# Kernel optimization log

Measured on AMD Instinct MI355X. Metric: run time of the kernel, lower is better.

The kernel has to match this reference:

```python
import jax, jax.numpy as jnp
import numpy as np

B, S, E, H = 4, 2048, 1024, 16
D = E // H  # head dim = 64


def setup_inputs() -> dict:
    key = jax.random.key(0)
    ks = jax.random.split(key, 9)
    sc = 1.0 / np.sqrt(E)
    x = jax.random.normal(ks[0], (B, S, E), dtype=jnp.float32)
    # causal mask: 1 = keep, 0 = masked -> -inf (matches masked_fill(mask==0, -inf))
    mask = jnp.broadcast_to(jnp.tril(jnp.ones((S, S), dtype=jnp.int32)), (B, S, S))
    return {
        "x": x,
        "mask": mask,
        "wq": jax.random.normal(ks[1], (E, E), dtype=jnp.float32) * sc,
        "bq": jax.random.normal(ks[2], (E,), dtype=jnp.float32) * sc,
        "wk": jax.random.normal(ks[3], (E, E), dtype=jnp.float32) * sc,
        "bk": jax.random.normal(ks[4], (E,), dtype=jnp.float32) * sc,
        "wv": jax.random.normal(ks[5], (E, E), dtype=jnp.float32) * sc,
        "bv": jax.random.normal(ks[6], (E,), dtype=jnp.float32) * sc,
        "wo": jax.random.normal(ks[7], (E, E), dtype=jnp.float32) * sc,
        "bo": jax.random.normal(ks[8], (E,), dtype=jnp.float32) * sc,
    }


def reference(x, mask, wq, bq, wk, bk, wv, bv, wo, bo):
    # nn.Linear: y = x @ W^T + b
    def proj(w, b):
        y = jnp.einsum('bse,fe->bsf', x, w) + b
        return y.reshape(B, S, H, D).transpose(0, 2, 1, 3)  # [B,H,S,D]

    q = proj(wq, bq)
    k = proj(wk, bk)
    v = proj(wv, bv)
    denom = jnp.asarray(np.sqrt(D), dtype=x.dtype)
    score = jnp.einsum('bhqd,bhkd->bhqk', q, k) / denom  # [B,H,S,S]
    score = jnp.where(mask[:, None, :, :] == 0, jnp.asarray(-jnp.inf, score.dtype), score)
    attn = jax.nn.softmax(score, axis=-1)
    out = jnp.einsum('bhqk,bhkd->bhqd', attn, v)  # [B,H,S,D]
    out = out.transpose(0, 2, 1, 3).reshape(B, S, E)
    return jnp.einsum('bse,fe->bsf', out, wo) + bo
```

## Files before the change

### kernel.cpp

```cpp
#include <hip/hip_runtime.h>
#include <cstdint>
#include <cstddef>

typedef unsigned short u16;
typedef __bf16 bf16;
typedef bf16 bf16x8 __attribute__((ext_vector_type(8)));
typedef bf16 bf16x4 __attribute__((ext_vector_type(4)));
typedef float f32x4 __attribute__((ext_vector_type(4)));
typedef u16 u16x8 __attribute__((ext_vector_type(8)));
typedef u16 u16x4 __attribute__((ext_vector_type(4)));

#define ASYNC16(g, l) __builtin_amdgcn_global_load_lds( \
    (const __attribute__((address_space(1))) void*)(g), \
    (__attribute__((address_space(3))) void*)(l), 16, 0, 0)

#define FENCE asm volatile("" ::: "memory")
#define BARRIER do { FENCE; __builtin_amdgcn_s_barrier(); FENCE; } while (0)
#define WAITVM(n) asm volatile("s_waitcnt vmcnt(" #n ")" ::: "memory")

__device__ __forceinline__ u16 f2bf(float f) {
  bf16 h = (bf16)f;
  return __builtin_bit_cast(u16, h);
}

__device__ __forceinline__ u16x4 pk4(float a, float b, float c, float d) {
  bf16x4 v = { (bf16)a, (bf16)b, (bf16)c, (bf16)d };
  return __builtin_bit_cast(u16x4, v);
}

__device__ __forceinline__ void store_out(u16* p, float v) { *p = f2bf(v); }
__device__ __forceinline__ void store_out(float* p, float v) { *p = v; }

__device__ __forceinline__ f32x4 mfma16(bf16x8 a, bf16x8 b, f32x4 c) {
  return __builtin_amdgcn_mfma_f32_16x16x32_bf16(a, b, c, 0, 0, 0);
}

__global__ void prep(const float* __restrict__ x,  const float* __restrict__ wq,
                     const float* __restrict__ wk, const float* __restrict__ wv,
                     const float* __restrict__ wo, const float* __restrict__ bq,
                     const float* __restrict__ bk,
                     u16* __restrict__ xb, u16* __restrict__ wqkb,
                     u16* __restrict__ wvb, u16* __restrict__ wob,
                     float* __restrict__ bqk, float scl)
{
  const int bid = blockIdx.x, tid = threadIdx.x;
  if (bid < 8192) {
    int i = bid * 256 + tid;
    float4 v = ((const float4*)x)[i];
    ((u16x4*)xb)[i] = pk4(v.x, v.y, v.z, v.w);
  } else if (bid < 12288) {
    int wsel = (bid - 8192) >> 10;
    int i = ((bid - 8192) & 1023) * 256 + tid;
    const float* src = wsel == 0 ? wq : wsel == 1 ? wk : wsel == 2 ? wv : wo;
    u16* dst = wsel == 0 ? wqkb : wsel == 1 ? wqkb + 1048576 : wsel == 2 ? wvb : wob;
    float s = wsel == 0 ? scl : 1.0f;
    float4 v = ((const float4*)src)[i];
    ((u16x4*)dst)[i] = pk4(v.x * s, v.y * s, v.z * s, v.w * s);
  } else {
    for (int i = tid; i < 1024; i += 256) {
      bqk[i] = bq[i] * scl;
      bqk[1024 + i] = bk[i];
    }
  }
}

template <typename OutT>
__device__ __forceinline__ void gemm128(
    u16* sA, u16* sB,
    const u16* __restrict__ A, const u16* __restrict__ Bm,
    const float* __restrict__ bias_col, const float* __restrict__ bias_row,
    OutT* __restrict__ C, int M, int N, int K, int bm, int bn)
{
  const int tid = threadIdx.x;
  const int w = tid >> 6, lane = tid & 63;
  const int quad = lane >> 4, l15 = lane & 15;
  const int wr = w >> 2, wc = w & 3;

  const int srow = tid >> 3;
  const int sslot = (tid & 7) ^ (srow & 7);
  const u16* gA = A + (size_t)(bm * 128 + srow) * K + sslot * 8;
  const u16* gB = Bm + (size_t)(bn * 256 + srow) * K + sslot * 8;
  u16* dA = sA + tid * 8;
  u16* dB = sB + tid * 8;
  const size_t rK64 = (size_t)64 * K;

  auto stage0 = [&](int c, int kt) {
    const u16* a = gA + kt * 64;
    u16* da = dA + c * 8192;
    ASYNC16(a, da);
    ASYNC16(a + rK64, da + 4096);
    ASYNC16(gB + kt * 64, dB + c * 16384);
  };
  auto stage1 = [&](int c, int kt) {
    const u16* b = gB + kt * 64;
    u16* db = dB + c * 16384;
    ASYNC16(b + rK64,     db + 4096);
    ASYNC16(b + 2 * rK64, db + 8192);
    ASYNC16(b + 3 * rK64, db + 12288);
  };

  f32x4 acc[4][4] = {};
  bf16x8 af[4][2];
  bf16x8 bfr[2][2];

  const int aRow = (wr * 64 + l15) * 64;
  const int bRow = (wc * 64 + l15) * 64;
  const int sw0 = (quad ^ (l15 & 7)) * 8;

#define LDA(SRC) do { \
    _Pragma("unroll") \
    for (int i = 0; i < 4; i++) { \
      af[i][0] = *(const bf16x8*)((SRC) + aRow + i * 1024 + sw0); \
      af[i][1] = *(const bf16x8*)((SRC) + aRow + i * 1024 + (sw0 ^ 32)); \
    } } while (0)

#define LDB(SRC, NH) do { \
    _Pragma("unroll") \
    for (int j = 0; j < 2; j++) { \
      bfr[j][0] = *(const bf16x8*)((SRC) + bRow + ((NH)*2 + j) * 1024 + sw0); \
      bfr[j][1] = *(const bf16x8*)((SRC) + bRow + ((NH)*2 + j) * 1024 + (sw0 ^ 32)); \
    } } while (0)

#define MMQ(NH) do { \
    __builtin_amdgcn_s_setprio(1); \
    _Pragma("unroll") \
    for (int i = 0; i < 4; i++) { \
      acc[i][(NH)*2+0] = mfma16(af[i][0], bfr[0][0], acc[i][(NH)*2+0]); \
      acc[i][(NH)*2+0] = mfma16(af[i][1], bfr[0][1], acc[i][(NH)*2+0]); \
      acc[i][(NH)*2+1] = mfma16(af[i][0], bfr[1][0], acc[i][(NH)*2+1]); \
      acc[i][(NH)*2+1] = mfma16(af[i][1], bfr[1][1], acc[i][(NH)*2+1]); \
    } \
    __builtin_amdgcn_s_setprio(0); \
  } while (0)

  const int NT = K >> 6;

  stage0(0, 0); stage1(0, 0);
  stage0(1, 1); stage1(1, 1);
  WAITVM(6);
  BARRIER;

  for (int t = 0; t < NT; ++t) {
    const int c = t % 3, c2 = (t + 2) % 3;
    const bool more = (t + 2 < NT);
    const u16* SA = sA + c * 8192;
    const u16* SB = sB + c * 16384;

    LDA(SA); LDB(SB, 0);
    if (more) stage0(c2, t + 2);
    BARRIER;
    MMQ(0);
    BARRIER;

    LDB(SB, 1);
    if (more) {
      stage1(c2, t + 2);
      WAITVM(6);
    } else if (t == NT - 2) {
      WAITVM(0);
    }
    BARRIER;
    MMQ(1);
    BARRIER;
  }

#pragma unroll
  for (int nh = 0; nh < 2; nh++) {
#pragma unroll
    for (int j = 0; j < 2; j++) {
      const int cc = bn * 256 + wc * 64 + nh * 32 + j * 16 + l15;
      const float bc = bias_col ? bias_col[cc] : 0.f;
#pragma unroll
      for (int i = 0; i < 4; i++) {
        const int r0 = bm * 128 + wr * 64 + i * 16 + quad * 4;
        f32x4 v = acc[i][nh * 2 + j];
#pragma unroll
        for (int ri = 0; ri < 4; ri++) {
          const float bb = bc + (bias_row ? bias_row[r0 + ri] : 0.f);
          store_out(&C[(size_t)(r0 + ri) * N + cc], v[ri] + bb);
        }
      }
    }
  }
#undef LDA
#undef LDB
#undef MMQ
}

__global__ __launch_bounds__(512, 2) void gemm_qkv(
    const u16* __restrict__ xb, const u16* __restrict__ wqkb,
    const u16* __restrict__ wvb, const float* __restrict__ bqk,
    const float* __restrict__ bv, u16* __restrict__ qk, u16* __restrict__ vt)
{
  __shared__ __align__(16) u16 sA[3 * 8192];
  __shared__ __align__(16) u16 sB[3 * 16384];
  const int id = blockIdx.x;
  if (id < 512) {
    gemm128<u16>(sA, sB, xb, wqkb, bqk, nullptr, qk, 8192, 2048, 1024,
                 id >> 3, id & 7);
  } else {
    const int j = id - 512;
    gemm128<u16>(sA, sB, wvb, xb, nullptr, bv, vt, 1024, 8192, 1024,
                 j & 7, j >> 3);
  }
}

__global__ __launch_bounds__(512, 2) void gemm_out(
    const u16* __restrict__ ctx, const u16* __restrict__ wob,
    const float* __restrict__ bo, float* __restrict__ out)
{
  __shared__ __align__(16) u16 sA[3 * 8192];
  __shared__ __align__(16) u16 sB[3 * 16384];
  const int id = blockIdx.x;
  gemm128<float>(sA, sB, ctx, wob, bo, nullptr, out, 8192, 1024, 1024,
                 id >> 2, id & 3);
}

__global__ __launch_bounds__(512, 2) void fattn(
    const u16* __restrict__ QK, const u16* __restrict__ VT, u16* __restrict__ ctx)
{
  __shared__ u16 Kt[128 * 64];
  __shared__ u16 Vt[64 * 128];
  __shared__ u16 Pt[8 * 32 * 64];

  const int tid = threadIdx.x;
  const int w = tid >> 6, lane = tid & 63;
  const int quad = lane >> 4, l15 = lane & 15;
  const int bx = blockIdx.x, h = blockIdx.y, b = blockIdx.z;
  const int P8[8] = {7, 0, 6, 1, 5, 2, 4, 3};
  const int tq = (b & 2) ? 7 - P8[bx] : P8[bx];
  const int qbase = tq * 256 + w * 32;

  const int kr = tid >> 3, kc = (tid & 7) ^ (kr & 7);
  const int vr = tid >> 4, vc = (tid & 15) ^ (vr & 15);

  const u16* QKb = QK + (size_t)b * 2048 * 2048;
  const u16* Kg = QKb + 1024 + h * 64 + kc * 8;
  const u16* Vg = VT + (size_t)(h * 64) * 8192 + b * 2048 + vc * 8;

  u16* Pw = Pt + w * 2048;

  bf16x8 ones;
#pragma unroll
  for (int j = 0; j < 8; j++) ones[j] = (bf16)1.0f;

  bf16x8 qf[2][2];
#pragma unroll
  for (int mt = 0; mt < 2; mt++)
#pragma unroll
    for (int ks = 0; ks < 2; ks++)
      qf[mt][ks] = *(const bf16x8*)(QKb + (size_t)(qbase + mt * 16 + l15) * 2048 +
                                    h * 64 + ks * 32 + quad * 8);

  f32x4 oacc[4][2] = {};
  f32x4 lacc[2] = {};

  const int tmax = 2 * tq + 1;
  for (int t = 0; t <= tmax; t++) {
    __syncthreads();
#pragma unroll
    for (int s = 0; s < 2; s++) {
      ASYNC16(Kg + (size_t)(t * 128 + s * 64 + kr) * 2048, Kt + (s * 512 + w * 64) * 8);
      ASYNC16(Vg + (size_t)(s * 32 + vr) * 8192 + t * 128,  Vt + (s * 512 + w * 64) * 8);
    }
    __syncthreads();

    f32x4 st[2][8] = {};
#pragma unroll
    for (int ks = 0; ks < 2; ks++) {
      bf16x8 kf[8];
#pragma unroll
      for (int nt = 0; nt < 8; nt++) {
        int row = nt * 16 + l15;
        kf[nt] = *(const bf16x8*)(Kt + (row * 8 + ((ks * 4 + quad) ^ (row & 7))) * 8);
      }
#pragma unroll
      for (int nt = 0; nt < 8; nt++) {
        st[0][nt] = mfma16(kf[nt], qf[0][ks], st[0][nt]);
        st[1][nt] = mfma16(kf[nt], qf[1][ks], st[1][nt]);
      }
    }

    if (t >= 2 * tq) {
#pragma unroll
      for (int mt = 0; mt < 2; mt++) {
        const int qg = qbase + mt * 16 + l15;
#pragma unroll
        for (int nt = 0; nt < 8; nt++)
#pragma unroll
          for (int r = 0; r < 4; r++)
            if (t * 128 + nt * 16 + quad * 4 + r > qg) st[mt][nt][r] = -3e38f;
      }
    }
#pragma unroll
    for (int mt = 0; mt < 2; mt++)
#pragma unroll
      for (int nt = 0; nt < 8; nt++)
#pragma unroll
        for (int r = 0; r < 4; r++)
          st[mt][nt][r] = exp2f(st[mt][nt][r]);

#pragma unroll
    for (int hf = 0; hf < 2; hf++) {
#pragma unroll
      for (int mt = 0; mt < 2; mt++) {
        const int row = mt * 16 + l15;
#pragma unroll
        for (int n2 = 0; n2 < 4; n2++) {
          int nt = hf * 4 + n2;
          u16x4 pk = pk4(st[mt][nt][0], st[mt][nt][1], st[mt][nt][2], st[mt][nt][3]);
          int c = n2 * 2 + (quad >> 1);
          *(u16x4*)(Pw + (row << 6) + ((c ^ (row & 7)) << 3) + ((quad & 1) << 2)) = pk;
        }
      }
#pragma unroll
      for (int ks = 0; ks < 2; ks++) {
        const int c = ks * 4 + quad;
        bf16x8 pf0 = *(const bf16x8*)(Pw + (l15 << 6) + ((c ^ (l15 & 7)) << 3));
        bf16x8 pf1 = *(const bf16x8*)(Pw + ((16 + l15) << 6) + ((c ^ (l15 & 7)) << 3));
        lacc[0] = mfma16(ones, pf0, lacc[0]);
        lacc[1] = mfma16(ones, pf1, lacc[1]);
#pragma unroll
        for (int dt = 0; dt < 4; dt++) {
          int row = dt * 16 + l15;
          bf16x8 vf = *(const bf16x8*)(Vt + (row * 16 + ((hf * 8 + ks * 4 + quad) ^ (row & 15))) * 8);
          oacc[dt][0] = mfma16(vf, pf0, oacc[dt][0]);
          oacc[dt][1] = mfma16(vf, pf1, oacc[dt][1]);
        }
      }
    }
  }

#pragma unroll
  for (int mt = 0; mt < 2; mt++) {
    float rl = 1.0f / lacc[mt][0];
    size_t row = (size_t)b * 2048 + qbase + mt * 16 + l15;
#pragma unroll
    for (int dt = 0; dt < 4; dt++) {
      u16x4 o = pk4(oacc[dt][mt][0] * rl, oacc[dt][mt][1] * rl,
                    oacc[dt][mt][2] * rl, oacc[dt][mt][3] * rl);
      *(u16x4*)(ctx + row * 1024 + h * 64 + dt * 16 + quad * 4) = o;
    }
  }
}

extern "C" void kernel_launch(void* const* d_in, const int* in_sizes, int n_in,
                              void* d_out, int out_size, void* d_ws, size_t ws_size,
                              hipStream_t stream)
{
  const float* x  = (const float*)d_in[0];
  const float* wq = (const float*)d_in[2];
  const float* bq = (const float*)d_in[3];
  const float* wk = (const float*)d_in[4];
  const float* bk = (const float*)d_in[5];
  const float* wv = (const float*)d_in[6];
  const float* bv = (const float*)d_in[7];
  const float* wo = (const float*)d_in[8];
  const float* bo = (const float*)d_in[9];

  const float SCL = 0.125f * 1.44269504088896f;

  char* ws = (char*)d_ws;
  u16*   xb   = (u16*)(ws);
  u16*   ctx  = (u16*)(ws);
  u16*   wqkb = (u16*)(ws + 16777216);
  u16*   wvb  = (u16*)(ws + 20971520);
  u16*   wob  = (u16*)(ws + 23068672);
  float* bqk  = (float*)(ws + 25165824);
  u16*   qk   = (u16*)(ws + 25174016);
  u16*   vt   = (u16*)(ws + 58728448);
  float* out  = (float*)d_out;

  prep<<<12289, 256, 0, stream>>>(x, wq, wk, wv, wo, bq, bk,
                                  xb, wqkb, wvb, wob, bqk, SCL);

  gemm_qkv<<<768, 512, 0, stream>>>(xb, wqkb, wvb, bqk, bv, qk, vt);
  fattn<<<dim3(8, 16, 4), 512, 0, stream>>>(qk, vt, ctx);
  gemm_out<<<256, 512, 0, stream>>>(ctx, wob, bo, out);
}
```

Before: 312.4 us.

## Double-buffer K/V tiles in flash attention and shrink per-warp P staging

```diff
diff --git a/kernel.cpp b/kernel.cpp
--- a/kernel.cpp
+++ b/kernel.cpp
@@ -219,9 +219,9 @@
 __global__ __launch_bounds__(512, 2) void fattn(
     const u16* __restrict__ QK, const u16* __restrict__ VT, u16* __restrict__ ctx)
 {
-  __shared__ u16 Kt[128 * 64];
-  __shared__ u16 Vt[64 * 128];
-  __shared__ u16 Pt[8 * 32 * 64];
+  __shared__ u16 Kt[2][128 * 64];
+  __shared__ u16 Vt[2][64 * 128];
+  __shared__ u16 Pt[8 * 32 * 32];
 
   const int tid = threadIdx.x;
   const int w = tid >> 6, lane = tid & 63;
@@ -238,7 +238,7 @@
   const u16* Kg = QKb + 1024 + h * 64 + kc * 8;
   const u16* Vg = VT + (size_t)(h * 64) * 8192 + b * 2048 + vc * 8;
 
-  u16* Pw = Pt + w * 2048;
+  u16* Pw = Pt + w * 1024;
 
   bf16x8 ones;
 #pragma unroll
@@ -252,18 +252,28 @@
       qf[mt][ks] = *(const bf16x8*)(QKb + (size_t)(qbase + mt * 16 + l15) * 2048 +
                                     h * 64 + ks * 32 + quad * 8);
 
+  auto stage = [&](int bi, int t) {
+#pragma unroll
+    for (int s = 0; s < 2; s++) {
+      ASYNC16(Kg + (size_t)(t * 128 + s * 64 + kr) * 2048, Kt[bi] + (s * 512 + w * 64) * 8);
+      ASYNC16(Vg + (size_t)(s * 32 + vr) * 8192 + t * 128,  Vt[bi] + (s * 512 + w * 64) * 8);
+    }
+  };
+
   f32x4 oacc[4][2] = {};
   f32x4 lacc[2] = {};
 
   const int tmax = 2 * tq + 1;
+  stage(0, 0);
+
   for (int t = 0; t <= tmax; t++) {
-    __syncthreads();
-#pragma unroll
-    for (int s = 0; s < 2; s++) {
-      ASYNC16(Kg + (size_t)(t * 128 + s * 64 + kr) * 2048, Kt + (s * 512 + w * 64) * 8);
-      ASYNC16(Vg + (size_t)(s * 32 + vr) * 8192 + t * 128,  Vt + (s * 512 + w * 64) * 8);
-    }
-    __syncthreads();
+    const int cur = t & 1;
+    if (t < tmax) { stage(cur ^ 1, t + 1); WAITVM(4); }
+    else          { WAITVM(0); }
+    BARRIER;
+
+    const u16* Kc = Kt[cur];
+    const u16* Vc = Vt[cur];
 
     f32x4 st[2][8] = {};
 #pragma unroll
@@ -272,7 +282,7 @@
 #pragma unroll
       for (int nt = 0; nt < 8; nt++) {
         int row = nt * 16 + l15;
-        kf[nt] = *(const bf16x8*)(Kt + (row * 8 + ((ks * 4 + quad) ^ (row & 7))) * 8);
+        kf[nt] = *(const bf16x8*)(Kc + (row * 8 + ((ks * 4 + quad) ^ (row & 7))) * 8);
       }
 #pragma unroll
       for (int nt = 0; nt < 8; nt++) {
@@ -303,32 +313,34 @@
 #pragma unroll
     for (int hf = 0; hf < 2; hf++) {
 #pragma unroll
-      for (int mt = 0; mt < 2; mt++) {
-        const int row = mt * 16 + l15;
-#pragma unroll
-        for (int n2 = 0; n2 < 4; n2++) {
-          int nt = hf * 4 + n2;
-          u16x4 pk = pk4(st[mt][nt][0], st[mt][nt][1], st[mt][nt][2], st[mt][nt][3]);
-          int c = n2 * 2 + (quad >> 1);
-          *(u16x4*)(Pw + (row << 6) + ((c ^ (row & 7)) << 3) + ((quad & 1) << 2)) = pk;
+      for (int ks = 0; ks < 2; ks++) {
+#pragma unroll
+        for (int mt = 0; mt < 2; mt++) {
+          const int row = mt * 16 + l15;
+          const int swz = (row >> 1) & 3;
+#pragma unroll
+          for (int j = 0; j < 2; j++) {
+            int nt = hf * 4 + ks * 2 + j;
+            u16x4 pkv = pk4(st[mt][nt][0], st[mt][nt][1], st[mt][nt][2], st[mt][nt][3]);
+            int c = (j * 2 + (quad >> 1)) ^ swz;
+            *(u16x4*)(Pw + (row << 5) + (c << 3) + ((quad & 1) << 2)) = pkv;
+          }
         }
-      }
-#pragma unroll
-      for (int ks = 0; ks < 2; ks++) {
-        const int c = ks * 4 + quad;
-        bf16x8 pf0 = *(const bf16x8*)(Pw + (l15 << 6) + ((c ^ (l15 & 7)) << 3));
-        bf16x8 pf1 = *(const bf16x8*)(Pw + ((16 + l15) << 6) + ((c ^ (l15 & 7)) << 3));
+        const int cq = quad ^ ((l15 >> 1) & 3);
+        bf16x8 pf0 = *(const bf16x8*)(Pw + (l15 << 5) + (cq << 3));
+        bf16x8 pf1 = *(const bf16x8*)(Pw + ((16 + l15) << 5) + (cq << 3));
         lacc[0] = mfma16(ones, pf0, lacc[0]);
         lacc[1] = mfma16(ones, pf1, lacc[1]);
 #pragma unroll
         for (int dt = 0; dt < 4; dt++) {
           int row = dt * 16 + l15;
-          bf16x8 vf = *(const bf16x8*)(Vt + (row * 16 + ((hf * 8 + ks * 4 + quad) ^ (row & 15))) * 8);
+          bf16x8 vf = *(const bf16x8*)(Vc + (row * 16 + ((hf * 8 + ks * 4 + quad) ^ (row & 15))) * 8);
           oacc[dt][0] = mfma16(vf, pf0, oacc[dt][0]);
           oacc[dt][1] = mfma16(vf, pf1, oacc[dt][1]);
         }
       }
     }
+    BARRIER;
   }
 
 #pragma unroll
```

New measurement: 313.9 us. Within noise of the previous version (+0.5%).
